# Kernel tuning notes

Hardware: AMD Instinct MI355X
Metric: run time of the kernel (lower is better)

## Reference

```python
import jax, jax.numpy as jnp
import numpy as np

B, S, H, NH = 2, 2048, 1024, 16
HD = H // NH


def setup_inputs() -> dict:
    key = jax.random.key(0)
    ks = jax.random.split(key, 12)
    inp = {
        "query": jax.random.normal(ks[0], (B, S, H), dtype=jnp.float32),
        "key": jax.random.normal(ks[1], (B, S, H), dtype=jnp.float32),
        "value": jax.random.normal(ks[2], (B, S, H), dtype=jnp.float32),
        "mask": jnp.ones((B, 1, S, S), dtype=jnp.int32),
        "script_mask": jax.random.uniform(ks[3], (B, S, S), dtype=jnp.float32),
    }
    scale = 1.0 / np.sqrt(H)
    inp["Wq"] = jax.random.normal(ks[4], (H, H), dtype=jnp.float32) * scale
    inp["bq"] = jnp.zeros((H,), dtype=jnp.float32)
    inp["Wk"] = jax.random.normal(ks[5], (H, H), dtype=jnp.float32) * scale
    inp["bk"] = jnp.zeros((H,), dtype=jnp.float32)
    inp["Wv"] = jax.random.normal(ks[6], (H, H), dtype=jnp.float32) * scale
    inp["bv"] = jnp.zeros((H,), dtype=jnp.float32)
    inp["Wo"] = jax.random.normal(ks[7], (H, H), dtype=jnp.float32) * scale
    inp["bo"] = jnp.zeros((H,), dtype=jnp.float32)
    return inp


def reference(query, key, value, mask, script_mask, Wq, bq, Wk, bk, Wv, bv, Wo, bo):
    b, s, h = query.shape
    # projections; torch Linear: x @ W.T + b
    q = (query @ Wq.T + bq).reshape(b, s, NH, HD).transpose(0, 2, 1, 3)  # [b,nh,s,hd]
    k = (key @ Wk.T + bk).reshape(b, s, NH, HD).transpose(0, 2, 1, 3)
    v = (value @ Wv.T + bv).reshape(b, s, NH, HD).transpose(0, 2, 1, 3)
    scores = jnp.einsum("bhqd,bhkd->bhqk", q, k) / jnp.sqrt(jnp.float32(HD))
    # multiplicative script mask, broadcast over heads
    scores = scores * script_mask[:, None, :, :]
    # additive mask: positions where mask == 0 -> -inf
    scores = jnp.where(mask == 0, -jnp.inf, scores)
    attn = jax.nn.softmax(scores, axis=-1)
    out = jnp.einsum("bhqk,bhkd->bhqd", attn, v)  # [b,nh,s,hd]
    out = out.transpose(0, 2, 1, 3).reshape(b, s, h)
    return out @ Wo.T + bo
```

## Files before the change

kernel.cpp:

```cpp
#include <hip/hip_runtime.h>
#include <stdint.h>

#define NH 16
#define SEQ 2048
#define HDIM 1024

typedef short bf16x8 __attribute__((ext_vector_type(8)));
typedef float f32x4 __attribute__((ext_vector_type(4)));

#define NEG_BIG (-1.0e30f)

static __device__ __forceinline__ uint32_t cvtpk_bf16(float lo, float hi) {
  uint32_t r;
  asm("v_cvt_pk_bf16_f32 %0, %1, %2" : "=v"(r) : "v"(lo), "v"(hi));
  return r;
}
static __device__ __forceinline__ uint16_t f2bf(float f) {
  return (uint16_t)cvtpk_bf16(f, f);
}

struct CvtArgs {
  const float* src[7];
  uint16_t* dst[7];
  int nblk[7];
};
__global__ __launch_bounds__(256) void cvt_bf16(CvtArgs a) {
  int ten = blockIdx.y;
  if (blockIdx.x >= a.nblk[ten]) return;
  size_t idx = ((size_t)blockIdx.x * 256 + threadIdx.x) * 8;
  const float* s = a.src[ten] + idx;
  float4 f0 = *(const float4*)(s);
  float4 f1 = *(const float4*)(s + 4);
  uint4 o;
  o.x = cvtpk_bf16(f0.x, f0.y);
  o.y = cvtpk_bf16(f0.z, f0.w);
  o.z = cvtpk_bf16(f1.x, f1.y);
  o.w = cvtpk_bf16(f1.z, f1.w);
  *(uint4*)(a.dst[ten] + idx) = o;
}

__global__ __launch_bounds__(256) void cm_prep(const int4* __restrict__ mask,
                                               const float4* __restrict__ sm,
                                               uint4* __restrict__ cm) {
  int i = blockIdx.x * 256 + threadIdx.x;
  int4 m0 = mask[2 * i];
  int4 m1 = mask[2 * i + 1];
  float4 s0 = sm[2 * i];
  float4 s1 = sm[2 * i + 1];
  const float cst = 0.18033688011112042f;
  auto pk = [&](int mA, int mB, float fa, float fb) -> uint32_t {
    float a = mA ? fa * cst : -1.0f;
    float b = mB ? fb * cst : -1.0f;
    return cvtpk_bf16(a, b);
  };
  uint4 o;
  o.x = pk(m0.x, m0.y, s0.x, s0.y);
  o.y = pk(m0.z, m0.w, s0.z, s0.w);
  o.z = pk(m1.x, m1.y, s1.x, s1.y);
  o.w = pk(m1.z, m1.w, s1.z, s1.w);
  cm[i] = o;
}

struct GemmArgs {
  const uint16_t* A[4];
  const uint16_t* B[4];
  const float* bias[4];
  void* C[4];
};

#define LDA 40

__global__ __launch_bounds__(256) void gemm_bt(GemmArgs ga, int modeBase) {
  int mode = modeBase + blockIdx.y;
  const uint16_t* __restrict__ A = ga.A[mode];
  const uint16_t* __restrict__ Bm = ga.B[mode];
  const float* __restrict__ bias = ga.bias[mode];

  int bid = blockIdx.x;
  int tm, tn;
  if (mode == 2) { tm = bid & 7; tn = bid >> 3; }
  else           { tm = bid >> 3; tn = bid & 7; }

  __shared__ uint16_t As[128 * LDA];
  __shared__ uint16_t Bs[128 * LDA];

  int t = threadIdx.x;
  int lane = t & 63, w = t >> 6;
  int quad = lane >> 4, lm = lane & 15;
  int wm = w >> 1, wn = w & 1;

  const uint16_t* Ab = A + (size_t)tm * 128 * 1024;
  const uint16_t* Bb = Bm + (size_t)tn * 128 * 1024;
  int srow = w * 32 + (lane >> 2);
  int scol = (lane & 3) * 8;

  f32x4 acc[4][4] = {};

  for (int kk = 0; kk < 1024; kk += 32) {
    uint4 a0 = *(const uint4*)(Ab + (size_t)srow * 1024 + kk + scol);
    uint4 a1 = *(const uint4*)(Ab + (size_t)(srow + 16) * 1024 + kk + scol);
    uint4 b0 = *(const uint4*)(Bb + (size_t)srow * 1024 + kk + scol);
    uint4 b1 = *(const uint4*)(Bb + (size_t)(srow + 16) * 1024 + kk + scol);
    __syncthreads();
    *(uint4*)&As[srow * LDA + scol] = a0;
    *(uint4*)&As[(srow + 16) * LDA + scol] = a1;
    *(uint4*)&Bs[srow * LDA + scol] = b0;
    *(uint4*)&Bs[(srow + 16) * LDA + scol] = b1;
    __syncthreads();

    bf16x8 af[4], bfr[4];
#pragma unroll
    for (int i = 0; i < 4; i++)
      af[i] = *(const bf16x8*)&As[(wm * 64 + i * 16 + lm) * LDA + quad * 8];
#pragma unroll
    for (int j = 0; j < 4; j++)
      bfr[j] = *(const bf16x8*)&Bs[(wn * 64 + j * 16 + lm) * LDA + quad * 8];
#pragma unroll
    for (int i = 0; i < 4; i++)
#pragma unroll
      for (int j = 0; j < 4; j++)
        acc[i][j] = __builtin_amdgcn_mfma_f32_16x16x32_bf16(af[i], bfr[j], acc[i][j], 0, 0, 0);
  }

  int rowb = tm * 128 + wm * 64;
  int colb = tn * 128 + wn * 64;
#pragma unroll
  for (int i = 0; i < 4; i++) {
#pragma unroll
    for (int j = 0; j < 4; j++) {
      int col = colb + j * 16 + lm;
#pragma unroll
      for (int r = 0; r < 4; r++) {
        int row = rowb + i * 16 + quad * 4 + r;
        float v = acc[i][j][r];
        if (mode == 2) {
          v += bias[row];
          int hh = row >> 6, hd = row & 63, b = col >> 11, s2 = col & 2047;
          ((uint16_t*)ga.C[2])[((size_t)((b * NH + hh) * 64 + hd) << 11) + s2] = f2bf(v);
        } else if (mode == 3) {
          v += bias[col];
          ((float*)ga.C[3])[(size_t)row * 1024 + col] = v;
        } else {
          v += bias[col];
          int b = row >> 11, s2 = row & 2047, hh = col >> 6, hd = col & 63;
          ((uint16_t*)ga.C[mode])[(((size_t)(b * NH + hh) * 2048 + s2) << 6) + hd] = f2bf(v);
        }
      }
    }
  }
}

#define LDK 72

__global__ __launch_bounds__(256) void attn(const uint16_t* __restrict__ qp,
                                            const uint16_t* __restrict__ kp,
                                            const uint16_t* __restrict__ vt,
                                            const uint16_t* __restrict__ cm,
                                            uint16_t* __restrict__ ao) {
  int h = blockIdx.x, qt = blockIdx.y, b = blockIdx.z;
  int t = threadIdx.x;
  int lane = t & 63, w = t >> 6;
  int quad = lane >> 4, c = lane & 15;

  __shared__ uint16_t Ks[64 * LDK];
  __shared__ uint16_t VTs[64 * LDK];
  __shared__ uint16_t Ps[64 * LDK];

  size_t bh = (size_t)(b * NH + h);
  const uint16_t* Kb = kp + bh * (SEQ * 64);
  const uint16_t* Vb = vt + bh * (64 * SEQ);
  const uint16_t* CMb = cm + ((size_t)b * SEQ + qt * 64) * SEQ;

  int qrow = qt * 64 + w * 16 + c;
  const uint16_t* Qb = qp + bh * (SEQ * 64) + (size_t)qrow * 64;
  bf16x8 qf0 = *(const bf16x8*)(Qb + quad * 8);
  bf16x8 qf1 = *(const bf16x8*)(Qb + 32 + quad * 8);

  f32x4 Oacc[4] = {};
  float m_run = NEG_BIG;
  float l_run = 0.0f;

  int krow = w * 8 + (lane >> 3);
  int kc = (lane & 7) * 8;

  const uint16_t* pK0 = Kb + (size_t)krow * 64 + kc;
  const uint16_t* pK1 = pK0 + 32 * 64;
  const uint16_t* pV0 = Vb + (size_t)krow * SEQ + kc;
  const uint16_t* pV1 = pV0 + (size_t)32 * SEQ;
  const uint16_t* pCM = CMb + (size_t)(w * 16 + c) * SEQ + quad * 4;

  uint16_t* sK0 = &Ks[krow * LDK + kc];
  uint16_t* sK1 = sK0 + 32 * LDK;
  uint16_t* sV0 = &VTs[krow * LDK + kc];
  uint16_t* sV1 = sV0 + 32 * LDK;

  const uint16_t* rK = &Ks[c * LDK];
  const uint16_t* rV = &VTs[c * LDK];
  uint16_t* sP = &Ps[(w * 16 + c) * LDK];
  int qo = quad * 8;

  for (int kt = 0; kt < SEQ; kt += 64) {
    uint2 cm0 = *(const uint2*)(pCM);
    uint2 cm1 = *(const uint2*)(pCM + 16);
    uint2 cm2 = *(const uint2*)(pCM + 32);
    uint2 cm3 = *(const uint2*)(pCM + 48);
    uint4 k0  = *(const uint4*)(pK0);
    uint4 k1  = *(const uint4*)(pK1);
    uint4 v0g = *(const uint4*)(pV0);
    uint4 v1g = *(const uint4*)(pV1);
    pCM += 64; pK0 += 64 * 64; pK1 += 64 * 64; pV0 += 64; pV1 += 64;
    __syncthreads();
    *(uint4*)sK0 = k0;
    *(uint4*)sK1 = k1;
    *(uint4*)sV0 = v0g;
    *(uint4*)sV1 = v1g;
    __syncthreads();

    f32x4 st[4];
    __builtin_amdgcn_s_setprio(1);
#pragma unroll
    for (int i = 0; i < 4; i++) {
      bf16x8 a0 = *(const bf16x8*)(rK + i * 16 * LDK + qo);
      bf16x8 a1 = *(const bf16x8*)(rK + i * 16 * LDK + 32 + qo);
      f32x4 z = {};
      z = __builtin_amdgcn_mfma_f32_16x16x32_bf16(a0, qf0, z, 0, 0, 0);
      st[i] = __builtin_amdgcn_mfma_f32_16x16x32_bf16(a1, qf1, z, 0, 0, 0);
    }
    __builtin_amdgcn_s_setprio(0);

    float p[16];
    float tmax = NEG_BIG;
    uint2 cmv[4] = {cm0, cm1, cm2, cm3};
#pragma unroll
    for (int i = 0; i < 4; i++) {
      uint32_t w0 = cmv[i].x, w1 = cmv[i].y;
      float cf[4];
      cf[0] = __builtin_bit_cast(float, w0 << 16);
      cf[1] = __builtin_bit_cast(float, w0 & 0xffff0000u);
      cf[2] = __builtin_bit_cast(float, w1 << 16);
      cf[3] = __builtin_bit_cast(float, w1 & 0xffff0000u);
#pragma unroll
      for (int r = 0; r < 4; r++) {
        float sv = st[i][r] * cf[r];
        sv = (cf[r] < 0.0f) ? NEG_BIG : sv;
        p[i * 4 + r] = sv;
      }
      tmax = fmaxf(tmax,
                   fmaxf(fmaxf(p[i * 4 + 0], p[i * 4 + 1]),
                         fmaxf(p[i * 4 + 2], p[i * 4 + 3])));
    }
    tmax = fmaxf(tmax, __shfl_xor(tmax, 16));
    tmax = fmaxf(tmax, __shfl_xor(tmax, 32));
    if (!__all(tmax <= m_run + 8.0f)) {
      float m_new = fmaxf(m_run, tmax);
      float alpha = exp2f(m_run - m_new);
      m_run = m_new;
      l_run *= alpha;
#pragma unroll
      for (int i = 0; i < 4; i++) Oacc[i] *= alpha;
    }
    float ls = 0.0f;
#pragma unroll
    for (int z2 = 0; z2 < 16; z2++) {
      p[z2] = exp2f(p[z2] - m_run);
      ls += p[z2];
    }
    l_run += ls;

#pragma unroll
    for (int i = 0; i < 4; i++) {
      uint2 pkd;
      pkd.x = cvtpk_bf16(p[i * 4 + 0], p[i * 4 + 1]);
      pkd.y = cvtpk_bf16(p[i * 4 + 2], p[i * 4 + 3]);
      *(uint2*)(sP + i * 16 + quad * 4) = pkd;
    }
    asm volatile("s_waitcnt lgkmcnt(0)" ::: "memory");
    __builtin_amdgcn_sched_barrier(0);

    bf16x8 pf0 = *(const bf16x8*)(sP + qo);
    bf16x8 pf1 = *(const bf16x8*)(sP + 32 + qo);
    __builtin_amdgcn_s_setprio(1);
#pragma unroll
    for (int i = 0; i < 4; i++) {
      bf16x8 v0 = *(const bf16x8*)(rV + i * 16 * LDK + qo);
      bf16x8 v1 = *(const bf16x8*)(rV + i * 16 * LDK + 32 + qo);
      Oacc[i] = __builtin_amdgcn_mfma_f32_16x16x32_bf16(v0, pf0, Oacc[i], 0, 0, 0);
      Oacc[i] = __builtin_amdgcn_mfma_f32_16x16x32_bf16(v1, pf1, Oacc[i], 0, 0, 0);
    }
    __builtin_amdgcn_s_setprio(0);
  }

  float lf = l_run + __shfl_xor(l_run, 16);
  lf = lf + __shfl_xor(lf, 32);
  float inv = 1.0f / lf;
  uint16_t* Ob = ao + ((size_t)(b * SEQ) + qt * 64 + w * 16 + c) * HDIM + h * 64;
#pragma unroll
  for (int i = 0; i < 4; i++) {
    uint2 ov;
    ov.x = cvtpk_bf16(Oacc[i][0] * inv, Oacc[i][1] * inv);
    ov.y = cvtpk_bf16(Oacc[i][2] * inv, Oacc[i][3] * inv);
    *(uint2*)(Ob + i * 16 + quad * 4) = ov;
  }
}

extern "C" void kernel_launch(void* const* d_in, const int* in_sizes, int n_in,
                              void* d_out, int out_size, void* d_ws, size_t ws_size,
                              hipStream_t stream) {
  (void)in_sizes; (void)n_in; (void)out_size; (void)ws_size;
  const float* query = (const float*)d_in[0];
  const float* key   = (const float*)d_in[1];
  const float* value = (const float*)d_in[2];
  const int*   mask  = (const int*)d_in[3];
  const float* smask = (const float*)d_in[4];
  const float* Wq = (const float*)d_in[5];
  const float* bq = (const float*)d_in[6];
  const float* Wk = (const float*)d_in[7];
  const float* bk = (const float*)d_in[8];
  const float* Wv = (const float*)d_in[9];
  const float* bv = (const float*)d_in[10];
  const float* Wo = (const float*)d_in[11];
  const float* bo = (const float*)d_in[12];

  char* p = (char*)d_ws;
  uint16_t* xq  = (uint16_t*)p; p += (size_t)2 * SEQ * HDIM * 2;
  uint16_t* xk  = (uint16_t*)p; p += (size_t)2 * SEQ * HDIM * 2;
  uint16_t* xv  = (uint16_t*)p; p += (size_t)2 * SEQ * HDIM * 2;
  uint16_t* wqb = (uint16_t*)p; p += (size_t)HDIM * HDIM * 2;
  uint16_t* wkb = (uint16_t*)p; p += (size_t)HDIM * HDIM * 2;
  uint16_t* wvb = (uint16_t*)p; p += (size_t)HDIM * HDIM * 2;
  uint16_t* wob = (uint16_t*)p; p += (size_t)HDIM * HDIM * 2;
  uint16_t* qp  = (uint16_t*)p; p += (size_t)2 * NH * SEQ * 64 * 2;
  uint16_t* kpp = (uint16_t*)p; p += (size_t)2 * NH * SEQ * 64 * 2;
  uint16_t* vtp = (uint16_t*)p; p += (size_t)2 * NH * SEQ * 64 * 2;
  uint16_t* cmw = (uint16_t*)p; p += (size_t)2 * SEQ * SEQ * 2;
  uint16_t* aob = (uint16_t*)p; p += (size_t)2 * SEQ * HDIM * 2;

  CvtArgs ca;
  ca.src[0] = query; ca.dst[0] = xq;  ca.nblk[0] = 2048;
  ca.src[1] = key;   ca.dst[1] = xk;  ca.nblk[1] = 2048;
  ca.src[2] = value; ca.dst[2] = xv;  ca.nblk[2] = 2048;
  ca.src[3] = Wq;    ca.dst[3] = wqb; ca.nblk[3] = 512;
  ca.src[4] = Wk;    ca.dst[4] = wkb; ca.nblk[4] = 512;
  ca.src[5] = Wv;    ca.dst[5] = wvb; ca.nblk[5] = 512;
  ca.src[6] = Wo;    ca.dst[6] = wob; ca.nblk[6] = 512;
  cvt_bf16<<<dim3(2048, 7), 256, 0, stream>>>(ca);

  cm_prep<<<4096, 256, 0, stream>>>((const int4*)mask, (const float4*)smask, (uint4*)cmw);

  GemmArgs ga;
  ga.A[0] = xq;  ga.B[0] = wqb; ga.bias[0] = bq; ga.C[0] = qp;
  ga.A[1] = xk;  ga.B[1] = wkb; ga.bias[1] = bk; ga.C[1] = kpp;
  ga.A[2] = wvb; ga.B[2] = xv;  ga.bias[2] = bv; ga.C[2] = vtp;
  ga.A[3] = aob; ga.B[3] = wob; ga.bias[3] = bo; ga.C[3] = d_out;

  gemm_bt<<<dim3(256, 3), 256, 0, stream>>>(ga, 0);
  attn<<<dim3(NH, SEQ / 64, 2), 256, 0, stream>>>(qp, kpp, vtp, cmw, aob);
  gemm_bt<<<dim3(256, 1), 256, 0, stream>>>(ga, 3);
}
```

Measured before the change: 367.5 us.

## Prefetch next K/V/mask tile into registers and use packed f32 softmax math

Restructures the attention key loop so the global loads for the next 64-key tile (K, V, script-mask) are issued before computing the current tile. This hides global-memory latency behind the MFMA and softmax work, using a manual two-stage unroll. It also rewrites the mask multiply and exp-sum with packed v_pk_mul/v_pk_add f32 instructions, and replaces the negative-mask select with a min against a scaled big constant. The cost is higher register pressure from the double-buffered operands, which may reduce occupancy.

```diff
diff --git a/kernel.cpp b/kernel.cpp
--- a/kernel.cpp
+++ b/kernel.cpp
@@ -7,6 +7,7 @@
 
 typedef short bf16x8 __attribute__((ext_vector_type(8)));
 typedef float f32x4 __attribute__((ext_vector_type(4)));
+typedef float f32x2 __attribute__((ext_vector_type(2)));
 
 #define NEG_BIG (-1.0e30f)
 
@@ -17,6 +18,19 @@
 }
 static __device__ __forceinline__ uint16_t f2bf(float f) {
   return (uint16_t)cvtpk_bf16(f, f);
+}
+static __device__ __forceinline__ f32x2 pk_mul(f32x2 a, f32x2 b) {
+  f32x2 d;
+  asm("v_pk_mul_f32 %0, %1, %2" : "=v"(d) : "v"(a), "v"(b));
+  return d;
+}
+static __device__ __forceinline__ f32x2 pk_add(f32x2 a, f32x2 b) {
+  f32x2 d;
+  asm("v_pk_add_f32 %0, %1, %2" : "=v"(d) : "v"(a), "v"(b));
+  return d;
+}
+static __device__ __forceinline__ float bitf(uint32_t u) {
+  return __builtin_bit_cast(float, u);
 }
 
 struct CvtArgs {
@@ -199,23 +213,7 @@
   uint16_t* sP = &Ps[(w * 16 + c) * LDK];
   int qo = quad * 8;
 
-  for (int kt = 0; kt < SEQ; kt += 64) {
-    uint2 cm0 = *(const uint2*)(pCM);
-    uint2 cm1 = *(const uint2*)(pCM + 16);
-    uint2 cm2 = *(const uint2*)(pCM + 32);
-    uint2 cm3 = *(const uint2*)(pCM + 48);
-    uint4 k0  = *(const uint4*)(pK0);
-    uint4 k1  = *(const uint4*)(pK1);
-    uint4 v0g = *(const uint4*)(pV0);
-    uint4 v1g = *(const uint4*)(pV1);
-    pCM += 64; pK0 += 64 * 64; pK1 += 64 * 64; pV0 += 64; pV1 += 64;
-    __syncthreads();
-    *(uint4*)sK0 = k0;
-    *(uint4*)sK1 = k1;
-    *(uint4*)sV0 = v0g;
-    *(uint4*)sV1 = v1g;
-    __syncthreads();
-
+  auto compute = [&](uint2 c0, uint2 c1, uint2 c2, uint2 c3) {
     f32x4 st[4];
     __builtin_amdgcn_s_setprio(1);
 #pragma unroll
@@ -228,26 +226,24 @@
     }
     __builtin_amdgcn_s_setprio(0);
 
-    float p[16];
+    const f32x2 big2 = {1.0e30f, 1.0e30f};
+    f32x2 pp[8];
     float tmax = NEG_BIG;
-    uint2 cmv[4] = {cm0, cm1, cm2, cm3};
+    const uint2 cmv[4] = {c0, c1, c2, c3};
 #pragma unroll
     for (int i = 0; i < 4; i++) {
       uint32_t w0 = cmv[i].x, w1 = cmv[i].y;
-      float cf[4];
-      cf[0] = __builtin_bit_cast(float, w0 << 16);
-      cf[1] = __builtin_bit_cast(float, w0 & 0xffff0000u);
-      cf[2] = __builtin_bit_cast(float, w1 << 16);
-      cf[3] = __builtin_bit_cast(float, w1 & 0xffff0000u);
-#pragma unroll
-      for (int r = 0; r < 4; r++) {
-        float sv = st[i][r] * cf[r];
-        sv = (cf[r] < 0.0f) ? NEG_BIG : sv;
-        p[i * 4 + r] = sv;
-      }
-      tmax = fmaxf(tmax,
-                   fmaxf(fmaxf(p[i * 4 + 0], p[i * 4 + 1]),
-                         fmaxf(p[i * 4 + 2], p[i * 4 + 3])));
+      f32x2 cf01 = {bitf(w0 << 16), bitf(w0 & 0xffff0000u)};
+      f32x2 cf23 = {bitf(w1 << 16), bitf(w1 & 0xffff0000u)};
+      f32x2 s01 = {st[i][0], st[i][1]};
+      f32x2 s23 = {st[i][2], st[i][3]};
+      f32x2 m01 = pk_mul(s01, cf01), q01 = pk_mul(big2, cf01);
+      f32x2 m23 = pk_mul(s23, cf23), q23 = pk_mul(big2, cf23);
+      f32x2 r01 = {fminf(m01.x, q01.x), fminf(m01.y, q01.y)};
+      f32x2 r23 = {fminf(m23.x, q23.x), fminf(m23.y, q23.y)};
+      pp[2 * i] = r01;
+      pp[2 * i + 1] = r23;
+      tmax = fmaxf(tmax, fmaxf(fmaxf(r01.x, r01.y), fmaxf(r23.x, r23.y)));
     }
     tmax = fmaxf(tmax, __shfl_xor(tmax, 16));
     tmax = fmaxf(tmax, __shfl_xor(tmax, 32));
@@ -259,19 +255,22 @@
 #pragma unroll
       for (int i = 0; i < 4; i++) Oacc[i] *= alpha;
     }
-    float ls = 0.0f;
-#pragma unroll
-    for (int z2 = 0; z2 < 16; z2++) {
-      p[z2] = exp2f(p[z2] - m_run);
-      ls += p[z2];
-    }
-    l_run += ls;
+    f32x2 mneg = {-m_run, -m_run};
+    f32x2 acc2 = {0.0f, 0.0f};
+#pragma unroll
+    for (int j = 0; j < 8; j++) {
+      f32x2 e = pk_add(pp[j], mneg);
+      pp[j].x = exp2f(e.x);
+      pp[j].y = exp2f(e.y);
+      acc2 = pk_add(acc2, pp[j]);
+    }
+    l_run += acc2.x + acc2.y;
 
 #pragma unroll
     for (int i = 0; i < 4; i++) {
       uint2 pkd;
-      pkd.x = cvtpk_bf16(p[i * 4 + 0], p[i * 4 + 1]);
-      pkd.y = cvtpk_bf16(p[i * 4 + 2], p[i * 4 + 3]);
+      pkd.x = cvtpk_bf16(pp[2 * i].x, pp[2 * i].y);
+      pkd.y = cvtpk_bf16(pp[2 * i + 1].x, pp[2 * i + 1].y);
       *(uint2*)(sP + i * 16 + quad * 4) = pkd;
     }
     asm volatile("s_waitcnt lgkmcnt(0)" ::: "memory");
@@ -288,6 +287,48 @@
       Oacc[i] = __builtin_amdgcn_mfma_f32_16x16x32_bf16(v1, pf1, Oacc[i], 0, 0, 0);
     }
     __builtin_amdgcn_s_setprio(0);
+  };
+
+  uint4 rk0 = *(const uint4*)(pK0), rk1 = *(const uint4*)(pK1);
+  uint4 rv0 = *(const uint4*)(pV0), rv1 = *(const uint4*)(pV1);
+  uint2 cA0 = *(const uint2*)(pCM);
+  uint2 cA1 = *(const uint2*)(pCM + 16);
+  uint2 cA2 = *(const uint2*)(pCM + 32);
+  uint2 cA3 = *(const uint2*)(pCM + 48);
+  pK0 += 64 * 64; pK1 += 64 * 64; pV0 += 64; pV1 += 64; pCM += 64;
+  uint2 cB0, cB1, cB2, cB3;
+
+  for (int it = 0; it < SEQ / 128; ++it) {
+    __syncthreads();
+    *(uint4*)sK0 = rk0;
+    *(uint4*)sK1 = rk1;
+    *(uint4*)sV0 = rv0;
+    *(uint4*)sV1 = rv1;
+    __syncthreads();
+    rk0 = *(const uint4*)(pK0); rk1 = *(const uint4*)(pK1);
+    rv0 = *(const uint4*)(pV0); rv1 = *(const uint4*)(pV1);
+    cB0 = *(const uint2*)(pCM);
+    cB1 = *(const uint2*)(pCM + 16);
+    cB2 = *(const uint2*)(pCM + 32);
+    cB3 = *(const uint2*)(pCM + 48);
+    pK0 += 64 * 64; pK1 += 64 * 64; pV0 += 64; pV1 += 64; pCM += 64;
+    compute(cA0, cA1, cA2, cA3);
+    __syncthreads();
+    *(uint4*)sK0 = rk0;
+    *(uint4*)sK1 = rk1;
+    *(uint4*)sV0 = rv0;
+    *(uint4*)sV1 = rv1;
+    __syncthreads();
+    if (it < SEQ / 128 - 1) {
+      rk0 = *(const uint4*)(pK0); rk1 = *(const uint4*)(pK1);
+      rv0 = *(const uint4*)(pV0); rv1 = *(const uint4*)(pV1);
+      cA0 = *(const uint2*)(pCM);
+      cA1 = *(const uint2*)(pCM + 16);
+      cA2 = *(const uint2*)(pCM + 32);
+      cA3 = *(const uint2*)(pCM + 48);
+      pK0 += 64 * 64; pK1 += 64 * 64; pV0 += 64; pV1 += 64; pCM += 64;
+    }
+    compute(cB0, cB1, cB2, cB3);
   }
 
   float lf = l_run + __shfl_xor(l_run, 16);
```

Result: slower. 390.4 us (+6.2%).

## Pipeline GEMM k-loop with direct global-to-LDS loads and triple buffering

Applied to the files above, without the earlier changes.

Replaces the register-staged global loads and double-sync LDS stores in the projection GEMM with direct global_load_lds transfers into a triple-buffered LDS ring. The next k-tile is prefetched while the current one is consumed, and a single barrier per iteration replaces two. This is meant to hide global memory latency and cut synchronisation overhead. In exchange, the LDS padding is removed, which may add bank conflicts on fragment reads, and correctness depends on the vmcnt counts matching the outstanding loads.

```diff
diff --git a/kernel.cpp b/kernel.cpp
--- a/kernel.cpp
+++ b/kernel.cpp
@@ -10,6 +10,9 @@
 
 #define NEG_BIG (-1.0e30f)
 
+static __device__ __forceinline__ float bf2f(uint32_t u) {
+  union { uint32_t u; float f; } v; v.u = u << 16; return v.f;
+}
 static __device__ __forceinline__ uint32_t cvtpk_bf16(float lo, float hi) {
   uint32_t r;
   asm("v_cvt_pk_bf16_f32 %0, %1, %2" : "=v"(r) : "v"(lo), "v"(hi));
@@ -17,6 +20,11 @@
 }
 static __device__ __forceinline__ uint16_t f2bf(float f) {
   return (uint16_t)cvtpk_bf16(f, f);
+}
+static __device__ __forceinline__ void gload_lds16(const void* g, void* l) {
+  __builtin_amdgcn_global_load_lds(
+      (const __attribute__((address_space(1))) void*)g,
+      (__attribute__((address_space(3))) void*)l, 16, 0, 0);
 }
 
 struct CvtArgs {
@@ -68,8 +76,6 @@
   void* C[4];
 };
 
-#define LDA 40
-
 __global__ __launch_bounds__(256) void gemm_bt(GemmArgs ga, int modeBase) {
   int mode = modeBase + blockIdx.y;
   const uint16_t* __restrict__ A = ga.A[mode];
@@ -81,8 +87,8 @@
   if (mode == 2) { tm = bid & 7; tn = bid >> 3; }
   else           { tm = bid >> 3; tn = bid & 7; }
 
-  __shared__ uint16_t As[128 * LDA];
-  __shared__ uint16_t Bs[128 * LDA];
+  __shared__ uint16_t As[3][128 * 32];
+  __shared__ uint16_t Bs[3][128 * 32];
 
   int t = threadIdx.x;
   int lane = t & 63, w = t >> 6;
@@ -91,35 +97,55 @@
 
   const uint16_t* Ab = A + (size_t)tm * 128 * 1024;
   const uint16_t* Bb = Bm + (size_t)tn * 128 * 1024;
-  int srow = w * 32 + (lane >> 2);
+
+  int srow = lane >> 2;
   int scol = (lane & 3) * 8;
+  const uint16_t* gA0 = Ab + (size_t)(w * 32 + srow) * 1024 + scol;
+  const uint16_t* gA1 = gA0 + 16 * 1024;
+  const uint16_t* gB0 = Bb + (size_t)(w * 32 + srow) * 1024 + scol;
+  const uint16_t* gB1 = gB0 + 16 * 1024;
+
+  uint16_t* rdA = As[0]; uint16_t* stA = As[1]; uint16_t* nxA = As[2];
+  uint16_t* rdB = Bs[0]; uint16_t* stB = Bs[1]; uint16_t* nxB = Bs[2];
+  int woff = w * 1024;
+
+  auto STAGE = [&](uint16_t* dA, uint16_t* dB) {
+    gload_lds16(gA0, dA + woff);
+    gload_lds16(gA1, dA + woff + 512);
+    gload_lds16(gB0, dB + woff);
+    gload_lds16(gB1, dB + woff + 512);
+    gA0 += 32; gA1 += 32; gB0 += 32; gB1 += 32;
+  };
 
   f32x4 acc[4][4] = {};
 
+  STAGE(rdA, rdB);
+
   for (int kk = 0; kk < 1024; kk += 32) {
-    uint4 a0 = *(const uint4*)(Ab + (size_t)srow * 1024 + kk + scol);
-    uint4 a1 = *(const uint4*)(Ab + (size_t)(srow + 16) * 1024 + kk + scol);
-    uint4 b0 = *(const uint4*)(Bb + (size_t)srow * 1024 + kk + scol);
-    uint4 b1 = *(const uint4*)(Bb + (size_t)(srow + 16) * 1024 + kk + scol);
-    __syncthreads();
-    *(uint4*)&As[srow * LDA + scol] = a0;
-    *(uint4*)&As[(srow + 16) * LDA + scol] = a1;
-    *(uint4*)&Bs[srow * LDA + scol] = b0;
-    *(uint4*)&Bs[(srow + 16) * LDA + scol] = b1;
-    __syncthreads();
+    if (kk + 32 < 1024) {
+      STAGE(stA, stB);
+      asm volatile("s_waitcnt vmcnt(4)" ::: "memory");
+    } else {
+      asm volatile("s_waitcnt vmcnt(0)" ::: "memory");
+    }
+    __builtin_amdgcn_s_barrier();
+    __builtin_amdgcn_sched_barrier(0);
 
     bf16x8 af[4], bfr[4];
 #pragma unroll
     for (int i = 0; i < 4; i++)
-      af[i] = *(const bf16x8*)&As[(wm * 64 + i * 16 + lm) * LDA + quad * 8];
+      af[i] = *(const bf16x8*)&rdA[(wm * 64 + i * 16 + lm) * 32 + quad * 8];
 #pragma unroll
     for (int j = 0; j < 4; j++)
-      bfr[j] = *(const bf16x8*)&Bs[(wn * 64 + j * 16 + lm) * LDA + quad * 8];
+      bfr[j] = *(const bf16x8*)&rdB[(wn * 64 + j * 16 + lm) * 32 + quad * 8];
 #pragma unroll
     for (int i = 0; i < 4; i++)
 #pragma unroll
       for (int j = 0; j < 4; j++)
         acc[i][j] = __builtin_amdgcn_mfma_f32_16x16x32_bf16(af[i], bfr[j], acc[i][j], 0, 0, 0);
+
+    uint16_t* tA = rdA; rdA = stA; stA = nxA; nxA = tA;
+    uint16_t* tB = rdB; rdB = stB; stB = nxB; nxB = tB;
   }
 
   int rowb = tm * 128 + wm * 64;
```

Result: faster. 343.2 us (-6.6%).
